# Optimization experiments

Hardware: AMD Instinct MI355X
Metric: run time of the kernel (lower is better)

Reference implementation:

```python
import math
import jax, jax.numpy as jnp
import numpy as np

EMBD_DIM = 1024
N_HEADS = 16
WINDOW = 9           # odd, per assert
STRIDE = WINDOW // 2 # 4
BS, T = 4, 4096      # t % stride == 0


def setup_inputs() -> dict:
    key = jax.random.key(0)
    ks = jax.random.split(key, 8)
    c = EMBD_DIM
    std = 0.02
    inp = {
        "q": jax.random.normal(ks[0], (BS, c, T), dtype=jnp.float32),
        "q_mask": jnp.ones((BS, 1, T), dtype=bool),
        # 1x1 Conv1d projections == pointwise linear: W (out, in), b (out,)
        "Wq": jax.random.normal(ks[1], (c, c), dtype=jnp.float32) * std,
        "bq": jnp.zeros((c,), dtype=jnp.float32),
        "Wk": jax.random.normal(ks[2], (c, c), dtype=jnp.float32) * std,
        "bk": jnp.zeros((c,), dtype=jnp.float32),
        "Wv": jax.random.normal(ks[3], (c, c), dtype=jnp.float32) * std,
        "bv": jnp.zeros((c,), dtype=jnp.float32),
        "Wp": jax.random.normal(ks[4], (c, c), dtype=jnp.float32) * std,
        "bp": jnp.zeros((c,), dtype=jnp.float32),
    }
    return inp


def _pointwise(x, W, b):
    # 1x1 Conv1d on (bs, c, t)
    return jnp.einsum('oc,bct->bot', W, x) + b[None, :, None]


def reference(q, q_mask, Wq, bq, Wk, bk, Wv, bv, Wp, bp):
    bs, c, t = q.shape
    h, w, s = N_HEADS, WINDOW, STRIDE
    d = c // h
    scale = 1.0 / math.sqrt(d)

    qq = _pointwise(q, Wq, bq)
    kk = _pointwise(q, Wk, bk)  # self-attention: k = v = q
    vv = _pointwise(q, Wv, bv)

    def split_heads(x):  # (bs, c, t) -> (bs*h, t, d)
        return x.reshape(bs, h, d, t).transpose(0, 1, 3, 2).reshape(bs * h, t, d)

    qh = split_heads(qq) * scale
    kh = split_heads(kk)
    vh = split_heads(vv)

    # Sliding-window indices: query i attends to keys j in [i-s, i+s].
    # This is exactly the band produced by the chunked as_strided code plus
    # its l_mask/r_mask boundary fills (which mask j < 0 and j >= t).
    offs = jnp.arange(-s, s + 1)                 # (w,)
    idx = jnp.arange(t)[:, None] + offs[None, :] # (t, w)
    in_range = (idx >= 0) & (idx < t)
    idxc = jnp.clip(idx, 0, t - 1)

    k_win = kh[:, idxc]                          # (bs*h, t, w, d)
    scores = jnp.einsum('ntd,ntwd->ntw', qh, k_win)
    scores = scores.reshape(bs, h, t, w)

    # kv mask: invalid key positions contribute -10000 (as in _attn_normalize)
    kv_valid = q_mask.reshape(bs, t)
    kv_bias = jnp.where(kv_valid[:, idxc], 0.0, -10000.0)  # (bs, t, w)
    scores = scores + kv_bias[:, None]
    scores = jnp.where(in_range[None, None], scores, -jnp.inf)

    attn = jax.nn.softmax(scores, axis=-1)
    # zero attention rows at invalid query positions
    attn = jnp.where(kv_valid[:, None, :, None], attn, 0.0)
    attn = attn.reshape(bs * h, t, w)

    v_win = vh[:, idxc]                          # (bs*h, t, w, d)
    out = jnp.einsum('ntw,ntwd->ntd', attn, v_win)

    out = out.reshape(bs, h, t, d).transpose(0, 1, 3, 2).reshape(bs, c, t)
    out = _pointwise(out, Wp, bp) * q_mask.astype(out.dtype)
    return (out, q_mask)
```

## Files before the change

### kernel.cpp

```cpp
#include <hip/hip_runtime.h>
#include <hip/hip_bf16.h>
#include <math.h>

#define T_SEQ 4096
#define C_DIM 1024
#define NH    16
#define HD    64
#define BSZ   4
#define VSTRIDE 4120
#define VPAD    12

typedef __attribute__((ext_vector_type(8))) short bf16x8;
typedef __attribute__((ext_vector_type(4))) float f32x4;

__device__ __forceinline__ unsigned short f2bf(float f) {
    union { __hip_bfloat16 h; unsigned short u; } cv;
    cv.h = __float2bfloat16(f);
    return cv.u;
}

__global__ __launch_bounds__(256) void conv_w_kernel(
    const float* __restrict__ Wq, const float* __restrict__ Wk,
    const float* __restrict__ Wv, const float* __restrict__ Wp,
    __hip_bfloat16* __restrict__ Wqkv, __hip_bfloat16* __restrict__ Wpb)
{
    int i = blockIdx.x * 256 + threadIdx.x;
    int which = i >> 18;
    int off = (i & 262143) << 2;
    const float* src = which == 0 ? Wq : which == 1 ? Wk : which == 2 ? Wv : Wp;
    float4 v = *reinterpret_cast<const float4*>(src + off);
    ushort4 o;
    o.x = f2bf(v.x); o.y = f2bf(v.y); o.z = f2bf(v.z); o.w = f2bf(v.w);
    __hip_bfloat16* dst = (which < 3) ? (Wqkv + ((size_t)which << 20) + off) : (Wpb + off);
    *reinterpret_cast<ushort4*>(dst) = o;
}

__global__ __launch_bounds__(256) void transpose_x_kernel(
    const float* __restrict__ q, __hip_bfloat16* __restrict__ xT)
{
    __shared__ float tile[64][65];
    int t0 = blockIdx.x * 64;
    int c0 = blockIdx.y * 64;
    int b  = blockIdx.z;
    int tx = threadIdx.x & 63;
    int ty = threadIdx.x >> 6;
    const float* src = q + ((size_t)b * C_DIM + c0) * T_SEQ + t0;
    #pragma unroll
    for (int i = 0; i < 16; ++i) {
        int c = ty + i * 4;
        tile[c][tx] = src[(size_t)c * T_SEQ + tx];
    }
    __syncthreads();
    __hip_bfloat16* dst = xT + ((size_t)b * T_SEQ + t0) * C_DIM + c0;
    #pragma unroll
    for (int i = 0; i < 16; ++i) {
        int t = ty + i * 4;
        dst[(size_t)t * C_DIM + tx] = __float2bfloat16(tile[tx][t]);
    }
}

__device__ __forceinline__ void stage_slot(
    const __hip_bfloat16* __restrict__ Ab, const __hip_bfloat16* __restrict__ Bb,
    __hip_bfloat16* As, __hip_bfloat16* Bs, int kbase, int tid, int wid)
{
    #pragma unroll
    for (int i = 0; i < 2; ++i) {
        int c = i * 512 + tid;
        int r = c >> 2;
        int sg = (c & 3) ^ ((r >> 1) & 3);
        const __hip_bfloat16* src = Ab + (size_t)r * C_DIM + kbase + sg * 8;
        __builtin_amdgcn_global_load_lds(
            (const __attribute__((address_space(1))) void*)src,
            (__attribute__((address_space(3))) void*)(As + (i * 512 + wid * 64) * 8),
            16, 0, 0);
    }
    {
        int c = tid;
        int r = c >> 2;
        int sg = (c & 3) ^ ((r >> 1) & 3);
        const __hip_bfloat16* src = Bb + (size_t)r * C_DIM + kbase + sg * 8;
        __builtin_amdgcn_global_load_lds(
            (const __attribute__((address_space(1))) void*)src,
            (__attribute__((address_space(3))) void*)(Bs + (wid * 64) * 8),
            16, 0, 0);
    }
}

#define GEMM_PIPELINE_CORE()                                                         \
    f32x4 acc[4][4] = {};                                                            \
    stage_slot(Abase, Bbase, Alds + 0 * 8192, Blds + 0 * 4096, 0, tid, wid);         \
    stage_slot(Abase, Bbase, Alds + 1 * 8192, Blds + 1 * 4096, 32, tid, wid);        \
    const int NST = C_DIM / 32;                                                      \
    int cs = 0;                                                                      \
    for (int st = 0; st < NST; ++st) {                                               \
        if (st == NST - 1)                                                           \
            asm volatile("s_waitcnt vmcnt(0)" ::: "memory");                         \
        else                                                                         \
            asm volatile("s_waitcnt vmcnt(3)" ::: "memory");                         \
        __builtin_amdgcn_s_barrier();                                                \
        if (st + 2 < NST) {                                                          \
            int ns = cs + 2; if (ns >= 3) ns -= 3;                                   \
            stage_slot(Abase, Bbase, Alds + ns * 8192, Blds + ns * 4096,             \
                       (st + 2) * 32, tid, wid);                                     \
        }                                                                            \
        const __hip_bfloat16* As = Alds + cs * 8192;                                 \
        const __hip_bfloat16* Bs = Blds + cs * 4096;                                 \
        bf16x8 af[4], bfr[4];                                                        \
        _Pragma("unroll")                                                            \
        for (int mi = 0; mi < 4; ++mi)                                               \
            af[mi] = *reinterpret_cast<const bf16x8*>(                               \
                As + (wr * 64 + mi * 16 + fr) * 32 + sof);                           \
        _Pragma("unroll")                                                            \
        for (int ni = 0; ni < 4; ++ni)                                               \
            bfr[ni] = *reinterpret_cast<const bf16x8*>(                              \
                Bs + (wc * 64 + ni * 16 + fr) * 32 + sof);                           \
        __builtin_amdgcn_s_setprio(1);                                               \
        _Pragma("unroll")                                                            \
        for (int mi = 0; mi < 4; ++mi) {                                             \
            _Pragma("unroll")                                                        \
            for (int ni = 0; ni < 4; ++ni)                                           \
                acc[mi][ni] = __builtin_amdgcn_mfma_f32_16x16x32_bf16(               \
                    af[mi], bfr[ni], acc[mi][ni], 0, 0, 0);                          \
        }                                                                            \
        __builtin_amdgcn_s_setprio(0);                                               \
        cs = cs + 1; if (cs == 3) cs = 0;                                            \
    }

__global__ __launch_bounds__(512, 4) void gemm_qkv_kernel(
    const __hip_bfloat16* __restrict__ A,
    const __hip_bfloat16* __restrict__ xT,
    const float* __restrict__ bq, const float* __restrict__ bk, const float* __restrict__ bv,
    __hip_bfloat16* __restrict__ qh, __hip_bfloat16* __restrict__ kh,
    __hip_bfloat16* __restrict__ vhT)
{
    __shared__ __align__(16) __hip_bfloat16 Alds[3 * 8192];
    __shared__ __align__(16) __hip_bfloat16 Blds[3 * 4096];
    int tid  = threadIdx.x;
    int lane = tid & 63;
    int wid  = tid >> 6;
    int wr = wid >> 1;
    int wc = wid & 1;
    int fr = lane & 15;
    int g  = lane >> 4;
    int sof = (g ^ ((fr >> 1) & 3)) * 8;

    const int NWG = 1536;
    int wg  = blockIdx.x;
    int swz = (wg & 7) * (NWG >> 3) + (wg >> 3);
    int n_i = swz & 31;
    int g2  = swz >> 5;
    int m_i = g2 % 12;
    int b   = g2 / 12;
    int n0 = n_i * 128;
    int m0 = m_i * 256;
    const __hip_bfloat16* Abase = A + (size_t)m0 * C_DIM;
    const __hip_bfloat16* Bbase = xT + ((size_t)b * T_SEQ + n0) * C_DIM;

    GEMM_PIPELINE_CORE()

    #pragma unroll
    for (int mi = 0; mi < 4; ++mi) {
        int mrow = m0 + wr * 64 + mi * 16 + g * 4;
        int which = mrow >> 10;
        int o = mrow & 1023;
        int hh = o >> 6, dd = o & 63;
        const float* bias = which == 0 ? bq : which == 1 ? bk : bv;
        float b0 = bias[o], b1 = bias[o + 1], b2 = bias[o + 2], b3 = bias[o + 3];
        if (which == 2) {
            size_t rowd = ((size_t)b * NH + hh) * HD + dd;
            #pragma unroll
            for (int ni = 0; ni < 4; ++ni) {
                int t = n0 + wc * 64 + ni * 16 + fr;
                vhT[(rowd + 0) * VSTRIDE + VPAD + t] = __float2bfloat16(acc[mi][ni][0] + b0);
                vhT[(rowd + 1) * VSTRIDE + VPAD + t] = __float2bfloat16(acc[mi][ni][1] + b1);
                vhT[(rowd + 2) * VSTRIDE + VPAD + t] = __float2bfloat16(acc[mi][ni][2] + b2);
                vhT[(rowd + 3) * VSTRIDE + VPAD + t] = __float2bfloat16(acc[mi][ni][3] + b3);
            }
        } else {
            __hip_bfloat16* outp = which == 0 ? qh : kh;
            size_t hb = ((size_t)b * NH + hh) * T_SEQ;
            #pragma unroll
            for (int ni = 0; ni < 4; ++ni) {
                int t = n0 + wc * 64 + ni * 16 + fr;
                ushort4 pk;
                pk.x = f2bf(acc[mi][ni][0] + b0);
                pk.y = f2bf(acc[mi][ni][1] + b1);
                pk.z = f2bf(acc[mi][ni][2] + b2);
                pk.w = f2bf(acc[mi][ni][3] + b3);
                *reinterpret_cast<ushort4*>(outp + (hb + t) * HD + dd) = pk;
            }
        }
    }
}

__global__ __launch_bounds__(512, 4) void gemm_proj_kernel(
    const __hip_bfloat16* __restrict__ A,
    const __hip_bfloat16* __restrict__ xT,
    const float* __restrict__ bp,
    const int* __restrict__ mask,
    float* __restrict__ out)
{
    __shared__ __align__(16) __hip_bfloat16 Alds[3 * 8192];
    __shared__ __align__(16) __hip_bfloat16 Blds[3 * 4096];
    int tid  = threadIdx.x;
    int lane = tid & 63;
    int wid  = tid >> 6;
    int wr = wid >> 1;
    int wc = wid & 1;
    int fr = lane & 15;
    int g  = lane >> 4;
    int sof = (g ^ ((fr >> 1) & 3)) * 8;

    int wg  = blockIdx.x;
    int swz = (wg & 7) * 64 + (wg >> 3);
    int n_i = swz & 31;
    int g2  = swz >> 5;
    int m_i = g2 & 3;
    int b   = g2 >> 2;
    int n0 = n_i * 128;
    int m0 = m_i * 256;
    const __hip_bfloat16* Abase = A + (size_t)m0 * C_DIM;
    const __hip_bfloat16* Bbase = xT + ((size_t)b * T_SEQ + n0) * C_DIM;

    GEMM_PIPELINE_CORE()

    #pragma unroll
    for (int mi = 0; mi < 4; ++mi) {
        int orow = m0 + wr * 64 + mi * 16 + g * 4;
        float b0 = bp[orow], b1 = bp[orow + 1], b2 = bp[orow + 2], b3 = bp[orow + 3];
        #pragma unroll
        for (int ni = 0; ni < 4; ++ni) {
            int t = n0 + wc * 64 + ni * 16 + fr;
            float mval = (mask[b * T_SEQ + t] != 0) ? 1.0f : 0.0f;
            size_t obase = ((size_t)b * C_DIM + orow) * T_SEQ + t;
            out[obase]             = (acc[mi][ni][0] + b0) * mval;
            out[obase + T_SEQ]     = (acc[mi][ni][1] + b1) * mval;
            out[obase + 2 * T_SEQ] = (acc[mi][ni][2] + b2) * mval;
            out[obase + 3 * T_SEQ] = (acc[mi][ni][3] + b3) * mval;
        }
    }
}

__global__ __launch_bounds__(256) void attn_kernel(
    const __hip_bfloat16* __restrict__ qh,
    const __hip_bfloat16* __restrict__ kh,
    const __hip_bfloat16* __restrict__ vhT,
    const int* __restrict__ mask,
    __hip_bfloat16* __restrict__ attnT)
{
    __shared__ __hip_bfloat16 Plds[4][16 * 40];
    int lane = threadIdx.x & 63;
    int wid  = threadIdx.x >> 6;
    int gw = blockIdx.x * 4 + wid;
    int bh = gw >> 7;
    int tg = gw & 127;
    int b = bh >> 4, h = bh & 15;
    size_t kqbase = (size_t)bh * T_SEQ * HD;
    const int* mrow = mask + b * T_SEQ;
    int fr = lane & 15;
    int g  = lane >> 4;
    char* pby = (char*)(&Plds[wid][0]);
    f32x4 zacc = {};

    for (int it = 0; it < 2; ++it) {
        int t0 = tg * 32 + it * 16;
        bf16x8 qB[2], kA[2][2];
        #pragma unroll
        for (int ks = 0; ks < 2; ++ks)
            qB[ks] = *reinterpret_cast<const bf16x8*>(qh + kqbase + (size_t)(t0 + fr) * HD + ks * 32 + g * 8);
        #pragma unroll
        for (int mt = 0; mt < 2; ++mt) {
            int kr = t0 - 4 + mt * 16 + fr;
            kr = min(max(kr, 0), T_SEQ - 1);
            #pragma unroll
            for (int ks = 0; ks < 2; ++ks)
                kA[mt][ks] = *reinterpret_cast<const bf16x8*>(kh + kqbase + (size_t)kr * HD + ks * 32 + g * 8);
        }
        f32x4 sacc[2] = {zacc, zacc};
        #pragma unroll
        for (int mt = 0; mt < 2; ++mt)
            #pragma unroll
            for (int ks = 0; ks < 2; ++ks)
                sacc[mt] = __builtin_amdgcn_mfma_f32_16x16x32_bf16(kA[mt][ks], qB[ks], sacc[mt], 0, 0, 0);

        float ev[2][4];
        float mx = -INFINITY;
        #pragma unroll
        for (int mt = 0; mt < 2; ++mt) {
            #pragma unroll
            for (int r = 0; r < 4; ++r) {
                int j = mt * 16 + g * 4 + r;
                int jg = t0 - 4 + j;
                int w = j - fr;
                int jc = min(max(jg, 0), T_SEQ - 1);
                float sv = sacc[mt][r] * 0.125f + (mrow[jc] != 0 ? 0.0f : -10000.0f);
                bool valid = (w >= 0) && (w <= 8) && (jg >= 0) && (jg < T_SEQ);
                ev[mt][r] = valid ? sv : -INFINITY;
                mx = fmaxf(mx, ev[mt][r]);
            }
        }
        mx = fmaxf(mx, __shfl_xor(mx, 16));
        mx = fmaxf(mx, __shfl_xor(mx, 32));
        float ss = 0.0f;
        #pragma unroll
        for (int mt = 0; mt < 2; ++mt) {
            #pragma unroll
            for (int r = 0; r < 4; ++r) {
                float e2 = __expf(ev[mt][r] - mx);
                ev[mt][r] = e2;
                ss += e2;
            }
        }
        ss += __shfl_xor(ss, 16);
        ss += __shfl_xor(ss, 32);
        float inv = 1.0f / ss;

        #pragma unroll
        for (int mt = 0; mt < 2; ++mt) {
            unsigned int lo = (unsigned int)f2bf(ev[mt][0] * inv) | ((unsigned int)f2bf(ev[mt][1] * inv) << 16);
            unsigned int hi = (unsigned int)f2bf(ev[mt][2] * inv) | ((unsigned int)f2bf(ev[mt][3] * inv) << 16);
            int jb = (mt * 16 + g * 4) * 2;
            *reinterpret_cast<unsigned int*>(pby + fr * 80 + jb)     = lo;
            *reinterpret_cast<unsigned int*>(pby + fr * 80 + jb + 4) = hi;
        }
        bf16x8 pB = *reinterpret_cast<const bf16x8*>(pby + fr * 80 + g * 16);

        int t = t0 + fr;
        float mq = (mrow[t] != 0) ? 1.0f : 0.0f;
        #pragma unroll
        for (int dt = 0; dt < 4; ++dt) {
            bf16x8 vA = *reinterpret_cast<const bf16x8*>(
                vhT + ((size_t)bh * HD + dt * 16 + fr) * VSTRIDE + VPAD + (t0 - 4) + g * 8);
            f32x4 o = __builtin_amdgcn_mfma_f32_16x16x32_bf16(vA, pB, zacc, 0, 0, 0);
            ushort4 pk;
            pk.x = f2bf(o[0] * mq);
            pk.y = f2bf(o[1] * mq);
            pk.z = f2bf(o[2] * mq);
            pk.w = f2bf(o[3] * mq);
            *reinterpret_cast<ushort4*>(attnT + ((size_t)b * T_SEQ + t) * C_DIM + h * HD + dt * 16 + g * 4) = pk;
        }
    }
}

__global__ __launch_bounds__(256) void mask_echo_kernel(
    const int* __restrict__ mask, float* __restrict__ out)
{
    int i = blockIdx.x * 256 + threadIdx.x;
    if (i < BSZ * T_SEQ) out[i] = (mask[i] != 0) ? 1.0f : 0.0f;
}

extern "C" void kernel_launch(void* const* d_in, const int* in_sizes, int n_in,
                              void* d_out, int out_size, void* d_ws, size_t ws_size,
                              hipStream_t stream)
{
    const float* q     = (const float*)d_in[0];
    const int*   qmask = (const int*)d_in[1];
    const float* Wq    = (const float*)d_in[2];
    const float* bq    = (const float*)d_in[3];
    const float* Wk    = (const float*)d_in[4];
    const float* bk    = (const float*)d_in[5];
    const float* Wv    = (const float*)d_in[6];
    const float* bv    = (const float*)d_in[7];
    const float* Wp    = (const float*)d_in[8];
    const float* bp    = (const float*)d_in[9];
    float* out = (float*)d_out;

    char* ws = (char*)d_ws;
    __hip_bfloat16* Wqkv  = (__hip_bfloat16*)(ws);
    __hip_bfloat16* Wpb   = (__hip_bfloat16*)(ws + 6291456);
    __hip_bfloat16* xT    = (__hip_bfloat16*)(ws + 8388608);
    __hip_bfloat16* attnT = (__hip_bfloat16*)(ws + 8388608);
    __hip_bfloat16* qh    = (__hip_bfloat16*)(ws + 41943040);
    __hip_bfloat16* kh    = (__hip_bfloat16*)(ws + 75497472);
    __hip_bfloat16* vhT   = (__hip_bfloat16*)(ws + 109051904);

    conv_w_kernel<<<4096, 256, 0, stream>>>(Wq, Wk, Wv, Wp, Wqkv, Wpb);
    transpose_x_kernel<<<dim3(64, 16, 4), 256, 0, stream>>>(q, xT);
    gemm_qkv_kernel<<<1536, 512, 0, stream>>>(Wqkv, xT, bq, bk, bv, qh, kh, vhT);
    attn_kernel<<<2048, 256, 0, stream>>>(qh, kh, vhT, qmask, attnT);
    gemm_proj_kernel<<<512, 512, 0, stream>>>(Wpb, attnT, bp, qmask, out);
    mask_echo_kernel<<<64, 256, 0, stream>>>(qmask, out + (size_t)BSZ * C_DIM * T_SEQ);
}
```

Measured before the change: 226.3 us.

## Shrink GEMM tiles to 128x128 with 256 threads and double-buffered LDS

Both GEMM kernels now use 128x128 output tiles with 4 waves (256 threads) instead of 256x128 with 8 waves. The workgroup count doubles, and LDS staging goes from a 3-slot prefetch-two-ahead ring to a 2-slot double buffer with an extra barrier per k-step. The aim is to raise occupancy and scheduling flexibility, at the cost of less A/B reuse per tile, shallower prefetch and more synchronisation.

```diff
diff --git a/kernel.cpp b/kernel.cpp
--- a/kernel.cpp
+++ b/kernel.cpp
@@ -61,50 +61,48 @@
 
 __device__ __forceinline__ void stage_slot(
     const __hip_bfloat16* __restrict__ Ab, const __hip_bfloat16* __restrict__ Bb,
-    __hip_bfloat16* As, __hip_bfloat16* Bs, int kbase, int tid, int wid)
+    __hip_bfloat16* As, __hip_bfloat16* Bs, int kbase, int tid)
 {
     #pragma unroll
     for (int i = 0; i < 2; ++i) {
-        int c = i * 512 + tid;
+        int c = i * 256 + tid;
         int r = c >> 2;
         int sg = (c & 3) ^ ((r >> 1) & 3);
         const __hip_bfloat16* src = Ab + (size_t)r * C_DIM + kbase + sg * 8;
         __builtin_amdgcn_global_load_lds(
             (const __attribute__((address_space(1))) void*)src,
-            (__attribute__((address_space(3))) void*)(As + (i * 512 + wid * 64) * 8),
+            (__attribute__((address_space(3))) void*)(As + c * 8),
             16, 0, 0);
     }
-    {
-        int c = tid;
+    #pragma unroll
+    for (int i = 0; i < 2; ++i) {
+        int c = i * 256 + tid;
         int r = c >> 2;
         int sg = (c & 3) ^ ((r >> 1) & 3);
         const __hip_bfloat16* src = Bb + (size_t)r * C_DIM + kbase + sg * 8;
         __builtin_amdgcn_global_load_lds(
             (const __attribute__((address_space(1))) void*)src,
-            (__attribute__((address_space(3))) void*)(Bs + (wid * 64) * 8),
+            (__attribute__((address_space(3))) void*)(Bs + c * 8),
             16, 0, 0);
     }
 }
 
 #define GEMM_PIPELINE_CORE()                                                         \
     f32x4 acc[4][4] = {};                                                            \
-    stage_slot(Abase, Bbase, Alds + 0 * 8192, Blds + 0 * 4096, 0, tid, wid);         \
-    stage_slot(Abase, Bbase, Alds + 1 * 8192, Blds + 1 * 4096, 32, tid, wid);        \
+    stage_slot(Abase, Bbase, Alds, Blds, 0, tid);                                    \
     const int NST = C_DIM / 32;                                                      \
-    int cs = 0;                                                                      \
     for (int st = 0; st < NST; ++st) {                                               \
-        if (st == NST - 1)                                                           \
+        int cur = st & 1;                                                            \
+        if (st + 1 < NST) {                                                          \
+            stage_slot(Abase, Bbase, Alds + (cur ^ 1) * 4096,                        \
+                       Blds + (cur ^ 1) * 4096, (st + 1) * 32, tid);                 \
+            asm volatile("s_waitcnt vmcnt(4)" ::: "memory");                         \
+        } else {                                                                     \
             asm volatile("s_waitcnt vmcnt(0)" ::: "memory");                         \
-        else                                                                         \
-            asm volatile("s_waitcnt vmcnt(3)" ::: "memory");                         \
+        }                                                                            \
         __builtin_amdgcn_s_barrier();                                                \
-        if (st + 2 < NST) {                                                          \
-            int ns = cs + 2; if (ns >= 3) ns -= 3;                                   \
-            stage_slot(Abase, Bbase, Alds + ns * 8192, Blds + ns * 4096,             \
-                       (st + 2) * 32, tid, wid);                                     \
-        }                                                                            \
-        const __hip_bfloat16* As = Alds + cs * 8192;                                 \
-        const __hip_bfloat16* Bs = Blds + cs * 4096;                                 \
+        const __hip_bfloat16* As = Alds + cur * 4096;                                \
+        const __hip_bfloat16* Bs = Blds + cur * 4096;                                \
         bf16x8 af[4], bfr[4];                                                        \
         _Pragma("unroll")                                                            \
         for (int mi = 0; mi < 4; ++mi)                                               \
@@ -123,18 +121,18 @@
                     af[mi], bfr[ni], acc[mi][ni], 0, 0, 0);                          \
         }                                                                            \
         __builtin_amdgcn_s_setprio(0);                                               \
-        cs = cs + 1; if (cs == 3) cs = 0;                                            \
-    }
-
-__global__ __launch_bounds__(512, 4) void gemm_qkv_kernel(
+        __builtin_amdgcn_s_barrier();                                                \
+    }
+
+__global__ __launch_bounds__(256, 4) void gemm_qkv_kernel(
     const __hip_bfloat16* __restrict__ A,
     const __hip_bfloat16* __restrict__ xT,
     const float* __restrict__ bq, const float* __restrict__ bk, const float* __restrict__ bv,
     __hip_bfloat16* __restrict__ qh, __hip_bfloat16* __restrict__ kh,
     __hip_bfloat16* __restrict__ vhT)
 {
-    __shared__ __align__(16) __hip_bfloat16 Alds[3 * 8192];
-    __shared__ __align__(16) __hip_bfloat16 Blds[3 * 4096];
+    __shared__ __align__(16) __hip_bfloat16 Alds[2 * 4096];
+    __shared__ __align__(16) __hip_bfloat16 Blds[2 * 4096];
     int tid  = threadIdx.x;
     int lane = tid & 63;
     int wid  = tid >> 6;
@@ -144,15 +142,15 @@
     int g  = lane >> 4;
     int sof = (g ^ ((fr >> 1) & 3)) * 8;
 
-    const int NWG = 1536;
+    const int NWG = 3072;
     int wg  = blockIdx.x;
     int swz = (wg & 7) * (NWG >> 3) + (wg >> 3);
     int n_i = swz & 31;
     int g2  = swz >> 5;
-    int m_i = g2 % 12;
-    int b   = g2 / 12;
+    int m_i = g2 % 24;
+    int b   = g2 / 24;
     int n0 = n_i * 128;
-    int m0 = m_i * 256;
+    int m0 = m_i * 128;
     const __hip_bfloat16* Abase = A + (size_t)m0 * C_DIM;
     const __hip_bfloat16* Bbase = xT + ((size_t)b * T_SEQ + n0) * C_DIM;
 
@@ -193,15 +191,15 @@
     }
 }
 
-__global__ __launch_bounds__(512, 4) void gemm_proj_kernel(
+__global__ __launch_bounds__(256, 4) void gemm_proj_kernel(
     const __hip_bfloat16* __restrict__ A,
     const __hip_bfloat16* __restrict__ xT,
     const float* __restrict__ bp,
     const int* __restrict__ mask,
     float* __restrict__ out)
 {
-    __shared__ __align__(16) __hip_bfloat16 Alds[3 * 8192];
-    __shared__ __align__(16) __hip_bfloat16 Blds[3 * 4096];
+    __shared__ __align__(16) __hip_bfloat16 Alds[2 * 4096];
+    __shared__ __align__(16) __hip_bfloat16 Blds[2 * 4096];
     int tid  = threadIdx.x;
     int lane = tid & 63;
     int wid  = tid >> 6;
@@ -212,13 +210,13 @@
     int sof = (g ^ ((fr >> 1) & 3)) * 8;
 
     int wg  = blockIdx.x;
-    int swz = (wg & 7) * 64 + (wg >> 3);
+    int swz = (wg & 7) * 128 + (wg >> 3);
     int n_i = swz & 31;
     int g2  = swz >> 5;
-    int m_i = g2 & 3;
-    int b   = g2 >> 2;
+    int m_i = g2 & 7;
+    int b   = g2 >> 3;
     int n0 = n_i * 128;
-    int m0 = m_i * 256;
+    int m0 = m_i * 128;
     const __hip_bfloat16* Abase = A + (size_t)m0 * C_DIM;
     const __hip_bfloat16* Bbase = xT + ((size_t)b * T_SEQ + n0) * C_DIM;
 
@@ -376,8 +374,8 @@
 
     conv_w_kernel<<<4096, 256, 0, stream>>>(Wq, Wk, Wv, Wp, Wqkv, Wpb);
     transpose_x_kernel<<<dim3(64, 16, 4), 256, 0, stream>>>(q, xT);
-    gemm_qkv_kernel<<<1536, 512, 0, stream>>>(Wqkv, xT, bq, bk, bv, qh, kh, vhT);
+    gemm_qkv_kernel<<<3072, 256, 0, stream>>>(Wqkv, xT, bq, bk, bv, qh, kh, vhT);
     attn_kernel<<<2048, 256, 0, stream>>>(qh, kh, vhT, qmask, attnT);
-    gemm_proj_kernel<<<512, 512, 0, stream>>>(Wpb, attnT, bp, qmask, out);
+    gemm_proj_kernel<<<1024, 256, 0, stream>>>(Wpb, attnT, bp, qmask, out);
     mask_echo_kernel<<<64, 256, 0, stream>>>(qmask, out + (size_t)BSZ * C_DIM * T_SEQ);
 }
```

Measured after the change: 240.4 us. 1.06x slower.
